# Kernel tuning notes

Hardware: AMD Instinct MI355X
Metric: run time of the kernel (lower is better)

Reference implementation:

```python
import jax, jax.numpy as jnp
import numpy as np

H = 64  # hidden_size hardcoded in the module


def _lstm_scan(x_pre, w_hh):
    # x_pre: [T, B, 4H] = x @ W_ih^T + b_ih + b_hh, precomputed for all steps
    # w_hh: [4H, H]. PyTorch gate order: i, f, g, o.
    B = x_pre.shape[1]
    h0 = jnp.zeros((B, H), x_pre.dtype)
    c0 = jnp.zeros((B, H), x_pre.dtype)

    def cell(carry, xp):
        h, c = carry
        gates = xp + h @ w_hh.T  # [B, 4H]
        i, f, g, o = jnp.split(gates, 4, axis=-1)
        i = jax.nn.sigmoid(i)
        f = jax.nn.sigmoid(f)
        g = jnp.tanh(g)
        o = jax.nn.sigmoid(o)
        c = f * c + i * g
        h = o * jnp.tanh(c)
        return (h, c), h

    _, hs = jax.lax.scan(cell, (h0, c0), x_pre)
    return hs  # [T, B, H]


def _bidir_layer(x, w_ih, w_hh, b_ih, b_hh):
    # x: [T, B, D]; w_ih: [2, 4H, D]; w_hh: [2, 4H, H]; b_*: [2, 4H]
    pre_f = jnp.einsum('tbd,gd->tbg', x, w_ih[0]) + b_ih[0] + b_hh[0]
    hs_f = _lstm_scan(pre_f, w_hh[0])
    xr = x[::-1]
    pre_b = jnp.einsum('tbd,gd->tbg', xr, w_ih[1]) + b_ih[1] + b_hh[1]
    hs_b = _lstm_scan(pre_b, w_hh[1])[::-1]  # re-reverse to align with time
    return jnp.concatenate([hs_f, hs_b], axis=-1)  # [T, B, 2H]


def setup_inputs() -> dict:
    key = jax.random.key(0)
    B, T, F = 1024, 512, 32
    ks = jax.random.split(key, 11)
    s = 1.0 / float(np.sqrt(H))  # PyTorch LSTM init: U(-1/sqrt(H), 1/sqrt(H))
    u = lambda k, shape: jax.random.uniform(k, shape, jnp.float32, -s, s)
    return dict(
        x=jax.random.normal(ks[0], (B, T, F), jnp.float32),
        w_ih0=u(ks[1], (2, 4 * H, F)),
        w_hh0=u(ks[2], (2, 4 * H, H)),
        b_ih0=u(ks[3], (2, 4 * H)),
        b_hh0=u(ks[4], (2, 4 * H)),
        w_ih1=u(ks[5], (2, 4 * H, 2 * H)),
        w_hh1=u(ks[6], (2, 4 * H, H)),
        b_ih1=u(ks[7], (2, 4 * H)),
        b_hh1=u(ks[8], (2, 4 * H)),
        fc_w=u(ks[9], (2, 2 * H)),
        fc_b=u(ks[10], (2,)),
    )


def reference(x, w_ih0, w_hh0, b_ih0, b_hh0, w_ih1, w_hh1, b_ih1, b_hh1, fc_w, fc_b):
    xt = jnp.transpose(x, (1, 0, 2))  # [T, B, F]
    h1 = _bidir_layer(xt, w_ih0, w_hh0, b_ih0, b_hh0)  # [T, B, 2H]
    h2 = _bidir_layer(h1, w_ih1, w_hh1, b_ih1, b_hh1)  # [T, B, 2H]
    last = h2[-1]  # out[:, -1, :] in batch_first layout -> [B, 2H]
    return last @ fc_w.T + fc_b  # [B, 2]
```

## Files before the change

kernel.cpp:

```cpp
#include <hip/hip_runtime.h>

#define TT 512
#define BB 1024
#define FF 32
#define HH 64
#define GG 256

__device__ float g_h1[(size_t)TT * BB * 2 * HH];
__device__ float g_pre0[(size_t)2 * TT * BB * GG];
__device__ float g_pre1[(size_t)TT * BB * GG];
__device__ float g_hf[(size_t)BB * HH];

__device__ __forceinline__ float fsigm(float x) {
    float e = __builtin_amdgcn_exp2f(x * -1.44269504088896f);
    return __builtin_amdgcn_rcpf(1.0f + e);
}
__device__ __forceinline__ float ftanh(float x) {
    float e = __builtin_amdgcn_exp2f(x * -2.88539008177793f);
    return 2.0f * __builtin_amdgcn_rcpf(1.0f + e) - 1.0f;
}
__device__ __forceinline__ float rlane(float v, int l) {
    return __int_as_float(__builtin_amdgcn_readlane(__float_as_int(v), l));
}

__global__ __launch_bounds__(256, 4) void pre_gemm0(
    const float* __restrict__ x,
    const float* __restrict__ w_ih,
    const float* __restrict__ b_ih,
    const float* __restrict__ b_hh)
{
    const int tid = threadIdx.x;
    const int b   = blockIdx.x >> 1;
    const int dir = blockIdx.x & 1;

    __shared__ __align__(16) float4 w4[8 * 256];
    __shared__ __align__(16) float xbuf[2][256];

    const float4* wsrc = (const float4*)(w_ih + ((size_t)dir * GG + tid) * FF);
#pragma unroll
    for (int kq = 0; kq < 8; ++kq) w4[kq * 256 + tid] = wsrc[kq];
    const float bias = b_ih[dir * GG + tid] + b_hh[dir * GG + tid];

    const float* xbase = x + (size_t)b * TT * FF;
    xbuf[0][tid] = xbase[tid];
    const size_t OS = (size_t)BB * GG;

    for (int tc = 0; tc < 64; ++tc) {
        const int cur = tc & 1;
        __syncthreads();

        float vnext = 0.f;
        if (tc + 1 < 64) vnext = xbase[(tc + 1) * 256 + tid];

        float a0 = bias, a1 = bias, a2 = bias, a3 = bias,
              a4 = bias, a5 = bias, a6 = bias, a7 = bias;
#pragma unroll
        for (int kq = 0; kq < 8; ++kq) {
            float4 wq = w4[kq * 256 + tid];
            const float4* xr = (const float4*)xbuf[cur];
            float4 q;
            q = xr[0 * 8 + kq]; a0 += q.x*wq.x + q.y*wq.y + q.z*wq.z + q.w*wq.w;
            q = xr[1 * 8 + kq]; a1 += q.x*wq.x + q.y*wq.y + q.z*wq.z + q.w*wq.w;
            q = xr[2 * 8 + kq]; a2 += q.x*wq.x + q.y*wq.y + q.z*wq.z + q.w*wq.w;
            q = xr[3 * 8 + kq]; a3 += q.x*wq.x + q.y*wq.y + q.z*wq.z + q.w*wq.w;
            q = xr[4 * 8 + kq]; a4 += q.x*wq.x + q.y*wq.y + q.z*wq.z + q.w*wq.w;
            q = xr[5 * 8 + kq]; a5 += q.x*wq.x + q.y*wq.y + q.z*wq.z + q.w*wq.w;
            q = xr[6 * 8 + kq]; a6 += q.x*wq.x + q.y*wq.y + q.z*wq.z + q.w*wq.w;
            q = xr[7 * 8 + kq]; a7 += q.x*wq.x + q.y*wq.y + q.z*wq.z + q.w*wq.w;
        }
        float* op = g_pre0 + (((size_t)dir * TT + tc * 8) * BB + b) * GG + tid;
        op[0] = a0; op[1 * OS] = a1; op[2 * OS] = a2; op[3 * OS] = a3;
        op[4 * OS] = a4; op[5 * OS] = a5; op[6 * OS] = a6; op[7 * OS] = a7;

        if (tc + 1 < 64) xbuf[1 - cur][tid] = vnext;
    }
}

template <int L>
__global__ __launch_bounds__(64, 1) void lstm_scan(
    const float* __restrict__ w_hh)
{
    const int l   = threadIdx.x;
    const int dir = (L == 0) ? (blockIdx.x & 1) : 0;
    const int b   = (L == 0) ? (int)(blockIdx.x >> 1) : (int)blockIdx.x;

    const float* wbase = w_hh + (size_t)dir * GG * HH;

    float4 wi[16], wf[16], wg[16], wo[16];
    {
        const float4* pi_ = (const float4*)(wbase + (size_t)(0   + l) * HH);
        const float4* pf_ = (const float4*)(wbase + (size_t)(64  + l) * HH);
        const float4* pg_ = (const float4*)(wbase + (size_t)(128 + l) * HH);
        const float4* po_ = (const float4*)(wbase + (size_t)(192 + l) * HH);
#pragma unroll
        for (int q = 0; q < 16; ++q) {
            wi[q] = pi_[q]; wf[q] = pf_[q]; wg[q] = pg_[q]; wo[q] = po_[q];
        }
    }

    const float* pre = (L == 0) ? (g_pre0 + (size_t)dir * TT * BB * GG) : g_pre1;

    float c = 0.f, h = 0.f;

    const int t0 = dir ? (TT - 1) : 0;
    const int t1 = dir ? (TT - 2) : 1;
    const float* pp0 = pre + ((size_t)t0 * BB + b) * GG;
    const float* pp1 = pre + ((size_t)t1 * BB + b) * GG;
    float ci0 = pp0[l], cf0 = pp0[64 + l], cg0 = pp0[128 + l], co0 = pp0[192 + l];
    float ci1 = pp1[l], cf1 = pp1[64 + l], cg1 = pp1[128 + l], co1 = pp1[192 + l];

    for (int s = 0; s < TT; ++s) {
        const int t = dir ? (TT - 1 - s) : s;

        float ni = 0.f, nf = 0.f, ng = 0.f, no_ = 0.f;
        if (s + 2 < TT) {
            const int tn = dir ? (TT - 3 - s) : (s + 2);
            const float* np = pre + ((size_t)tn * BB + b) * GG;
            ni = np[l]; nf = np[64 + l]; ng = np[128 + l]; no_ = np[192 + l];
        }

        float ai = ci0, af = cf0, ag = cg0, ao = co0;

#define STEPQ(q) do {                                                        \
        float s0 = rlane(h, 4*(q)+0), s1 = rlane(h, 4*(q)+1),                \
              s2 = rlane(h, 4*(q)+2), s3 = rlane(h, 4*(q)+3);                \
        ai += s0*wi[q].x + s1*wi[q].y + s2*wi[q].z + s3*wi[q].w;             \
        af += s0*wf[q].x + s1*wf[q].y + s2*wf[q].z + s3*wf[q].w;             \
        ag += s0*wg[q].x + s1*wg[q].y + s2*wg[q].z + s3*wg[q].w;             \
        ao += s0*wo[q].x + s1*wo[q].y + s2*wo[q].z + s3*wo[q].w;             \
    } while (0)

        STEPQ(0);  STEPQ(1);  STEPQ(2);  STEPQ(3);
        STEPQ(4);  STEPQ(5);  STEPQ(6);  STEPQ(7);
        STEPQ(8);  STEPQ(9);  STEPQ(10); STEPQ(11);
        STEPQ(12); STEPQ(13); STEPQ(14); STEPQ(15);
#undef STEPQ

        const float ig = fsigm(ai);
        const float fg = fsigm(af);
        const float gg = ftanh(ag);
        const float og = fsigm(ao);
        c = fg * c + ig * gg;
        h = og * ftanh(c);

        if (L == 0) {
            g_h1[((size_t)t * BB + b) * (2 * HH) + dir * HH + l] = h;
        } else {
            if (s == TT - 1) g_hf[(size_t)b * HH + l] = h;
        }

        ci0 = ci1; cf0 = cf1; cg0 = cg1; co0 = co1;
        ci1 = ni;  cf1 = nf;  cg1 = ng;  co1 = no_;
    }
}

__global__ __launch_bounds__(256, 2) void pre_gemm1(
    const float* __restrict__ w_ih,
    const float* __restrict__ b_ih,
    const float* __restrict__ b_hh)
{
    const int tid  = threadIdx.x;
    const int gl   = tid & 127;
    const int rg   = tid >> 7;
    const int b    = blockIdx.x >> 1;
    const int gate = (blockIdx.x & 1) * 128 + gl;

    __shared__ __align__(16) float4 w4[28 * 128];
    __shared__ __align__(16) float4 hstg[2][8 * 32];

    const float4* wsrc = (const float4*)w_ih + (size_t)gate * 32;
#pragma unroll
    for (int i = 0; i < 14; ++i) {
        int kq = rg * 14 + i;
        w4[kq * 128 + gl] = wsrc[kq];
    }
    float4 wr0 = wsrc[28], wr1 = wsrc[29], wr2 = wsrc[30], wr3 = wsrc[31];
    const float bias = b_ih[gate] + b_hh[gate];

    const int srow = tid >> 5, sq = tid & 31;
    hstg[0][srow * 32 + sq] =
        *((const float4*)(g_h1 + ((size_t)srow * BB + b) * 128) + sq);

    const size_t RS = (size_t)BB * GG;

    for (int tc = 0; tc < 64; ++tc) {
        const int cur = tc & 1;
        __syncthreads();

        float4 vnext = make_float4(0.f, 0.f, 0.f, 0.f);
        if (tc + 1 < 64)
            vnext = *((const float4*)(g_h1 +
                      ((size_t)((tc + 1) * 8 + srow) * BB + b) * 128) + sq);

        const float4* hr0 = &hstg[cur][(rg * 4 + 0) * 32];
        const float4* hr1 = &hstg[cur][(rg * 4 + 1) * 32];
        const float4* hr2 = &hstg[cur][(rg * 4 + 2) * 32];
        const float4* hr3 = &hstg[cur][(rg * 4 + 3) * 32];

        float a0 = bias, a1 = bias, a2 = bias, a3 = bias;
#pragma unroll
        for (int kq = 0; kq < 28; ++kq) {
            float4 wq = w4[kq * 128 + gl];
            float4 q;
            q = hr0[kq]; a0 += q.x*wq.x + q.y*wq.y + q.z*wq.z + q.w*wq.w;
            q = hr1[kq]; a1 += q.x*wq.x + q.y*wq.y + q.z*wq.z + q.w*wq.w;
            q = hr2[kq]; a2 += q.x*wq.x + q.y*wq.y + q.z*wq.z + q.w*wq.w;
            q = hr3[kq]; a3 += q.x*wq.x + q.y*wq.y + q.z*wq.z + q.w*wq.w;
        }
        {
            float4 q;
            q = hr0[28]; a0 += q.x*wr0.x + q.y*wr0.y + q.z*wr0.z + q.w*wr0.w;
            q = hr1[28]; a1 += q.x*wr0.x + q.y*wr0.y + q.z*wr0.z + q.w*wr0.w;
            q = hr2[28]; a2 += q.x*wr0.x + q.y*wr0.y + q.z*wr0.z + q.w*wr0.w;
            q = hr3[28]; a3 += q.x*wr0.x + q.y*wr0.y + q.z*wr0.z + q.w*wr0.w;
            q = hr0[29]; a0 += q.x*wr1.x + q.y*wr1.y + q.z*wr1.z + q.w*wr1.w;
            q = hr1[29]; a1 += q.x*wr1.x + q.y*wr1.y + q.z*wr1.z + q.w*wr1.w;
            q = hr2[29]; a2 += q.x*wr1.x + q.y*wr1.y + q.z*wr1.z + q.w*wr1.w;
            q = hr3[29]; a3 += q.x*wr1.x + q.y*wr1.y + q.z*wr1.z + q.w*wr1.w;
            q = hr0[30]; a0 += q.x*wr2.x + q.y*wr2.y + q.z*wr2.z + q.w*wr2.w;
            q = hr1[30]; a1 += q.x*wr2.x + q.y*wr2.y + q.z*wr2.z + q.w*wr2.w;
            q = hr2[30]; a2 += q.x*wr2.x + q.y*wr2.y + q.z*wr2.z + q.w*wr2.w;
            q = hr3[30]; a3 += q.x*wr2.x + q.y*wr2.y + q.z*wr2.z + q.w*wr2.w;
            q = hr0[31]; a0 += q.x*wr3.x + q.y*wr3.y + q.z*wr3.z + q.w*wr3.w;
            q = hr1[31]; a1 += q.x*wr3.x + q.y*wr3.y + q.z*wr3.z + q.w*wr3.w;
            q = hr2[31]; a2 += q.x*wr3.x + q.y*wr3.y + q.z*wr3.z + q.w*wr3.w;
            q = hr3[31]; a3 += q.x*wr3.x + q.y*wr3.y + q.z*wr3.z + q.w*wr3.w;
        }
        {
            const int tb = tc * 8 + rg * 4;
            float* op = g_pre1 + ((size_t)tb * BB + b) * GG + gate;
            op[0 * RS] = a0; op[1 * RS] = a1; op[2 * RS] = a2; op[3 * RS] = a3;
        }
        if (tc + 1 < 64) hstg[1 - cur][srow * 32 + sq] = vnext;
    }
}

#define FMAC4(W, P0, P1, P2, P3, K) do{                                   \
    float4 v_;                                                           \
    v_ = (P0)[K]; acc0 += W.x*v_.x; acc0 += W.y*v_.y; acc0 += W.z*v_.z; acc0 += W.w*v_.w; \
    v_ = (P1)[K]; acc1 += W.x*v_.x; acc1 += W.y*v_.y; acc1 += W.z*v_.z; acc1 += W.w*v_.w; \
    v_ = (P2)[K]; acc2 += W.x*v_.x; acc2 += W.y*v_.y; acc2 += W.z*v_.z; acc2 += W.w*v_.w; \
    v_ = (P3)[K]; acc3 += W.x*v_.x; acc3 += W.y*v_.y; acc3 += W.z*v_.z; acc3 += W.w*v_.w; \
}while(0)

__global__ __launch_bounds__(256, 2) void lstm_final(
    const float* __restrict__ w_ih,
    const float* __restrict__ b_ih,
    const float* __restrict__ b_hh,
    const float* __restrict__ fc_w,
    const float* __restrict__ fc_b,
    float* __restrict__ out)
{
    const int tid = threadIdx.x;
    const int b0  = blockIdx.x * 4;

    __shared__ __align__(16) float x_lds[4][128];
    __shared__ __align__(16) float gact[4][GG];
    __shared__ __align__(16) float last[4][128];

#pragma unroll
    for (int r = 0; r < 2; ++r) {
        int idx = tid + r * 256;
        int b = idx >> 7, col = idx & 127;
        x_lds[b][col] = g_h1[((size_t)(TT - 1) * BB + (b0 + b)) * 128 + col];
    }

    const float4* p = (const float4*)(w_ih + ((size_t)GG + tid) * 128);
    float4 w0 = p[0],  w1 = p[1],  w2 = p[2],  w3 = p[3],  w4 = p[4],  w5 = p[5],
           w6 = p[6],  w7 = p[7],  w8 = p[8],  w9 = p[9],  w10 = p[10], w11 = p[11],
           w12 = p[12], w13 = p[13], w14 = p[14], w15 = p[15], w16 = p[16], w17 = p[17],
           w18 = p[18], w19 = p[19], w20 = p[20], w21 = p[21], w22 = p[22], w23 = p[23],
           w24 = p[24], w25 = p[25], w26 = p[26], w27 = p[27], w28 = p[28], w29 = p[29],
           w30 = p[30], w31 = p[31];
    const float bias = b_ih[GG + tid] + b_hh[GG + tid];
    __syncthreads();

    const float4* xb0 = (const float4*)x_lds[0];
    const float4* xb1 = (const float4*)x_lds[1];
    const float4* xb2 = (const float4*)x_lds[2];
    const float4* xb3 = (const float4*)x_lds[3];

    float acc0 = bias, acc1 = bias, acc2 = bias, acc3 = bias;
    FMAC4(w0, xb0, xb1, xb2, xb3, 0);   FMAC4(w1, xb0, xb1, xb2, xb3, 1);
    FMAC4(w2, xb0, xb1, xb2, xb3, 2);   FMAC4(w3, xb0, xb1, xb2, xb3, 3);
    FMAC4(w4, xb0, xb1, xb2, xb3, 4);   FMAC4(w5, xb0, xb1, xb2, xb3, 5);
    FMAC4(w6, xb0, xb1, xb2, xb3, 6);   FMAC4(w7, xb0, xb1, xb2, xb3, 7);
    FMAC4(w8, xb0, xb1, xb2, xb3, 8);   FMAC4(w9, xb0, xb1, xb2, xb3, 9);
    FMAC4(w10, xb0, xb1, xb2, xb3, 10); FMAC4(w11, xb0, xb1, xb2, xb3, 11);
    FMAC4(w12, xb0, xb1, xb2, xb3, 12); FMAC4(w13, xb0, xb1, xb2, xb3, 13);
    FMAC4(w14, xb0, xb1, xb2, xb3, 14); FMAC4(w15, xb0, xb1, xb2, xb3, 15);
    FMAC4(w16, xb0, xb1, xb2, xb3, 16); FMAC4(w17, xb0, xb1, xb2, xb3, 17);
    FMAC4(w18, xb0, xb1, xb2, xb3, 18); FMAC4(w19, xb0, xb1, xb2, xb3, 19);
    FMAC4(w20, xb0, xb1, xb2, xb3, 20); FMAC4(w21, xb0, xb1, xb2, xb3, 21);
    FMAC4(w22, xb0, xb1, xb2, xb3, 22); FMAC4(w23, xb0, xb1, xb2, xb3, 23);
    FMAC4(w24, xb0, xb1, xb2, xb3, 24); FMAC4(w25, xb0, xb1, xb2, xb3, 25);
    FMAC4(w26, xb0, xb1, xb2, xb3, 26); FMAC4(w27, xb0, xb1, xb2, xb3, 27);
    FMAC4(w28, xb0, xb1, xb2, xb3, 28); FMAC4(w29, xb0, xb1, xb2, xb3, 29);
    FMAC4(w30, xb0, xb1, xb2, xb3, 30); FMAC4(w31, xb0, xb1, xb2, xb3, 31);

    const bool is_g = ((tid >> 6) == 2);
    gact[0][tid] = is_g ? ftanh(acc0) : fsigm(acc0);
    gact[1][tid] = is_g ? ftanh(acc1) : fsigm(acc1);
    gact[2][tid] = is_g ? ftanh(acc2) : fsigm(acc2);
    gact[3][tid] = is_g ? ftanh(acc3) : fsigm(acc3);
    __syncthreads();

    {
        const int cb = tid >> 6, cj = tid & 63;
        float ig = gact[cb][cj];
        float gg = gact[cb][2 * HH + cj];
        float og = gact[cb][3 * HH + cj];
        float c = ig * gg;
        float h = og * ftanh(c);
        last[cb][HH + cj] = h;
        last[cb][cj] = g_hf[(size_t)(b0 + cb) * HH + cj];
    }
    __syncthreads();

    if (tid < 8) {
        int b = tid >> 1, o = tid & 1;
        float a = fc_b[o];
#pragma unroll
        for (int j = 0; j < 128; ++j) a += fc_w[o * 128 + j] * last[b][j];
        out[(size_t)(b0 + b) * 2 + o] = a;
    }
}

extern "C" void kernel_launch(void* const* d_in, const int* in_sizes, int n_in,
                              void* d_out, int out_size, void* d_ws, size_t ws_size,
                              hipStream_t stream) {
    const float* x     = (const float*)d_in[0];
    const float* w_ih0 = (const float*)d_in[1];
    const float* w_hh0 = (const float*)d_in[2];
    const float* b_ih0 = (const float*)d_in[3];
    const float* b_hh0 = (const float*)d_in[4];
    const float* w_ih1 = (const float*)d_in[5];
    const float* w_hh1 = (const float*)d_in[6];
    const float* b_ih1 = (const float*)d_in[7];
    const float* b_hh1 = (const float*)d_in[8];
    const float* fc_w  = (const float*)d_in[9];
    const float* fc_b  = (const float*)d_in[10];
    float* out = (float*)d_out;

    pre_gemm0<<<2048, 256, 0, stream>>>(x, w_ih0, b_ih0, b_hh0);
    lstm_scan<0><<<2048, 64, 0, stream>>>(w_hh0);
    pre_gemm1<<<2048, 256, 0, stream>>>(w_ih1, b_ih1, b_hh1);
    lstm_scan<1><<<1024, 64, 0, stream>>>(w_hh1);
    lstm_final<<<256, 256, 0, stream>>>(w_ih1, b_ih1, b_hh1, fc_w, fc_b, out);
}
```

Baseline: 2.623 ms.

## Rewrite layer-1 input projection as shared-memory tiled GEMM; relax scan launch bounds

Replaces the per-batch-row pre_gemm1, which kept weights in LDS and walked time in chunks, with a standard 64x64 output-tile GEMM over the flattened (T*B) x 128 activations. Each thread computes a 4x4 register tile from padded LDS tiles, and the grid grows to cover all tiles. The aim is better data reuse and parallelism in the projection. The trade-off is that the weight tile is reloaded and transposed into LDS by every block. Separately, the lstm_scan launch bound now allows 2 blocks per SIMD, which may constrain register allocation for the 64 float4 weight registers and risks spills.

```diff
diff --git a/kernel.cpp b/kernel.cpp
--- a/kernel.cpp
+++ b/kernel.cpp
@@ -77,7 +77,7 @@
 }
 
 template <int L>
-__global__ __launch_bounds__(64, 1) void lstm_scan(
+__global__ __launch_bounds__(64, 2) void lstm_scan(
     const float* __restrict__ w_hh)
 {
     const int l   = threadIdx.x;
@@ -154,85 +154,75 @@
     }
 }
 
+#define FMA4(c, s, b) do { c.x += (s)*(b).x; c.y += (s)*(b).y; \
+                           c.z += (s)*(b).z; c.w += (s)*(b).w; } while (0)
+
 __global__ __launch_bounds__(256, 2) void pre_gemm1(
     const float* __restrict__ w_ih,
     const float* __restrict__ b_ih,
     const float* __restrict__ b_hh)
 {
-    const int tid  = threadIdx.x;
-    const int gl   = tid & 127;
-    const int rg   = tid >> 7;
-    const int b    = blockIdx.x >> 1;
-    const int gate = (blockIdx.x & 1) * 128 + gl;
-
-    __shared__ __align__(16) float4 w4[28 * 128];
-    __shared__ __align__(16) float4 hstg[2][8 * 32];
-
-    const float4* wsrc = (const float4*)w_ih + (size_t)gate * 32;
-#pragma unroll
-    for (int i = 0; i < 14; ++i) {
-        int kq = rg * 14 + i;
-        w4[kq * 128 + gl] = wsrc[kq];
-    }
-    float4 wr0 = wsrc[28], wr1 = wsrc[29], wr2 = wsrc[30], wr3 = wsrc[31];
-    const float bias = b_ih[gate] + b_hh[gate];
-
-    const int srow = tid >> 5, sq = tid & 31;
-    hstg[0][srow * 32 + sq] =
-        *((const float4*)(g_h1 + ((size_t)srow * BB + b) * 128) + sq);
-
-    const size_t RS = (size_t)BB * GG;
-
-    for (int tc = 0; tc < 64; ++tc) {
-        const int cur = tc & 1;
-        __syncthreads();
-
-        float4 vnext = make_float4(0.f, 0.f, 0.f, 0.f);
-        if (tc + 1 < 64)
-            vnext = *((const float4*)(g_h1 +
-                      ((size_t)((tc + 1) * 8 + srow) * BB + b) * 128) + sq);
-
-        const float4* hr0 = &hstg[cur][(rg * 4 + 0) * 32];
-        const float4* hr1 = &hstg[cur][(rg * 4 + 1) * 32];
-        const float4* hr2 = &hstg[cur][(rg * 4 + 2) * 32];
-        const float4* hr3 = &hstg[cur][(rg * 4 + 3) * 32];
-
-        float a0 = bias, a1 = bias, a2 = bias, a3 = bias;
-#pragma unroll
-        for (int kq = 0; kq < 28; ++kq) {
-            float4 wq = w4[kq * 128 + gl];
-            float4 q;
-            q = hr0[kq]; a0 += q.x*wq.x + q.y*wq.y + q.z*wq.z + q.w*wq.w;
-            q = hr1[kq]; a1 += q.x*wq.x + q.y*wq.y + q.z*wq.z + q.w*wq.w;
-            q = hr2[kq]; a2 += q.x*wq.x + q.y*wq.y + q.z*wq.z + q.w*wq.w;
-            q = hr3[kq]; a3 += q.x*wq.x + q.y*wq.y + q.z*wq.z + q.w*wq.w;
-        }
-        {
-            float4 q;
-            q = hr0[28]; a0 += q.x*wr0.x + q.y*wr0.y + q.z*wr0.z + q.w*wr0.w;
-            q = hr1[28]; a1 += q.x*wr0.x + q.y*wr0.y + q.z*wr0.z + q.w*wr0.w;
-            q = hr2[28]; a2 += q.x*wr0.x + q.y*wr0.y + q.z*wr0.z + q.w*wr0.w;
-            q = hr3[28]; a3 += q.x*wr0.x + q.y*wr0.y + q.z*wr0.z + q.w*wr0.w;
-            q = hr0[29]; a0 += q.x*wr1.x + q.y*wr1.y + q.z*wr1.z + q.w*wr1.w;
-            q = hr1[29]; a1 += q.x*wr1.x + q.y*wr1.y + q.z*wr1.z + q.w*wr1.w;
-            q = hr2[29]; a2 += q.x*wr1.x + q.y*wr1.y + q.z*wr1.z + q.w*wr1.w;
-            q = hr3[29]; a3 += q.x*wr1.x + q.y*wr1.y + q.z*wr1.z + q.w*wr1.w;
-            q = hr0[30]; a0 += q.x*wr2.x + q.y*wr2.y + q.z*wr2.z + q.w*wr2.w;
-            q = hr1[30]; a1 += q.x*wr2.x + q.y*wr2.y + q.z*wr2.z + q.w*wr2.w;
-            q = hr2[30]; a2 += q.x*wr2.x + q.y*wr2.y + q.z*wr2.z + q.w*wr2.w;
-            q = hr3[30]; a3 += q.x*wr2.x + q.y*wr2.y + q.z*wr2.z + q.w*wr2.w;
-            q = hr0[31]; a0 += q.x*wr3.x + q.y*wr3.y + q.z*wr3.z + q.w*wr3.w;
-            q = hr1[31]; a1 += q.x*wr3.x + q.y*wr3.y + q.z*wr3.z + q.w*wr3.w;
-            q = hr2[31]; a2 += q.x*wr3.x + q.y*wr3.y + q.z*wr3.z + q.w*wr3.w;
-            q = hr3[31]; a3 += q.x*wr3.x + q.y*wr3.y + q.z*wr3.z + q.w*wr3.w;
-        }
-        {
-            const int tb = tc * 8 + rg * 4;
-            float* op = g_pre1 + ((size_t)tb * BB + b) * GG + gate;
-            op[0 * RS] = a0; op[1 * RS] = a1; op[2 * RS] = a2; op[3 * RS] = a3;
-        }
-        if (tc + 1 < 64) hstg[1 - cur][srow * 32 + sq] = vnext;
-    }
+    __shared__ __align__(16) float As[64 * 132];
+    __shared__ __align__(16) float Bs[128 * 68];
+
+    const int tid   = threadIdx.x;
+    const int mbase = (int)(blockIdx.x >> 2) * 64;
+    const int n0    = (int)(blockIdx.x & 3) * 64;
+
+#pragma unroll
+    for (int i = 0; i < 8; ++i) {
+        const int qid = tid + 256 * i;
+        const int r = qid >> 5, q = qid & 31;
+        float4 v = *(const float4*)(g_h1 + (size_t)(mbase + r) * 128 + q * 4);
+        *(float4*)(&As[r * 132 + q * 4]) = v;
+    }
+#pragma unroll
+    for (int i = 0; i < 8; ++i) {
+        const int qid = tid + 256 * i;
+        const int r = qid >> 5, q = qid & 31;
+        float4 v = *(const float4*)(w_ih + (size_t)(n0 + r) * 128 + q * 4);
+        Bs[(q * 4 + 0) * 68 + r] = v.x;
+        Bs[(q * 4 + 1) * 68 + r] = v.y;
+        Bs[(q * 4 + 2) * 68 + r] = v.z;
+        Bs[(q * 4 + 3) * 68 + r] = v.w;
+    }
+    __syncthreads();
+
+    const int tx = tid & 15, ty = tid >> 4;
+
+    float4 c0 = make_float4(0.f, 0.f, 0.f, 0.f);
+    float4 c1 = c0, c2 = c0, c3 = c0;
+
+#pragma unroll 8
+    for (int kq = 0; kq < 32; ++kq) {
+        const float4 a0 = *(const float4*)&As[(ty * 4 + 0) * 132 + kq * 4];
+        const float4 a1 = *(const float4*)&As[(ty * 4 + 1) * 132 + kq * 4];
+        const float4 a2 = *(const float4*)&As[(ty * 4 + 2) * 132 + kq * 4];
+        const float4 a3 = *(const float4*)&As[(ty * 4 + 3) * 132 + kq * 4];
+        const float4 b0 = *(const float4*)&Bs[(kq * 4 + 0) * 68 + tx * 4];
+        const float4 b1 = *(const float4*)&Bs[(kq * 4 + 1) * 68 + tx * 4];
+        const float4 b2 = *(const float4*)&Bs[(kq * 4 + 2) * 68 + tx * 4];
+        const float4 b3 = *(const float4*)&Bs[(kq * 4 + 3) * 68 + tx * 4];
+        FMA4(c0, a0.x, b0); FMA4(c0, a0.y, b1); FMA4(c0, a0.z, b2); FMA4(c0, a0.w, b3);
+        FMA4(c1, a1.x, b0); FMA4(c1, a1.y, b1); FMA4(c1, a1.z, b2); FMA4(c1, a1.w, b3);
+        FMA4(c2, a2.x, b0); FMA4(c2, a2.y, b1); FMA4(c2, a2.z, b2); FMA4(c2, a2.w, b3);
+        FMA4(c3, a3.x, b0); FMA4(c3, a3.y, b1); FMA4(c3, a3.z, b2); FMA4(c3, a3.w, b3);
+    }
+
+    float4 bias4;
+    bias4.x = b_ih[n0 + tx * 4 + 0] + b_hh[n0 + tx * 4 + 0];
+    bias4.y = b_ih[n0 + tx * 4 + 1] + b_hh[n0 + tx * 4 + 1];
+    bias4.z = b_ih[n0 + tx * 4 + 2] + b_hh[n0 + tx * 4 + 2];
+    bias4.w = b_ih[n0 + tx * 4 + 3] + b_hh[n0 + tx * 4 + 3];
+
+    FMA4(c0, 1.f, bias4); FMA4(c1, 1.f, bias4);
+    FMA4(c2, 1.f, bias4); FMA4(c3, 1.f, bias4);
+
+    float* ob = g_pre1 + (size_t)(mbase + ty * 4) * GG + n0 + tx * 4;
+    *(float4*)(ob + 0 * (size_t)GG) = c0;
+    *(float4*)(ob + 1 * (size_t)GG) = c1;
+    *(float4*)(ob + 2 * (size_t)GG) = c2;
+    *(float4*)(ob + 3 * (size_t)GG) = c3;
 }
 
 #define FMAC4(W, P0, P1, P2, P3, K) do{                                   \
@@ -344,7 +334,7 @@
 
     pre_gemm0<<<2048, 256, 0, stream>>>(x, w_ih0, b_ih0, b_hh0);
     lstm_scan<0><<<2048, 64, 0, stream>>>(w_hh0);
-    pre_gemm1<<<2048, 256, 0, stream>>>(w_ih1, b_ih1, b_hh1);
+    pre_gemm1<<<32768, 256, 0, stream>>>(w_ih1, b_ih1, b_hh1);
     lstm_scan<1><<<1024, 64, 0, stream>>>(w_hh1);
     lstm_final<<<256, 256, 0, stream>>>(w_ih1, b_ih1, b_hh1, fc_w, fc_b, out);
 }
```

Result: slower. 3.943 ms (+50.3%).
